# Kernel tuning notes

Hardware: AMD Instinct MI355X
Metric: run time of the kernel (lower is better)

The kernel has to match this reference:

```python
import jax, jax.numpy as jnp
import numpy as np
from jax import lax

NH = 1024
CATS = 1024
B = 64
T = 512


def setup_inputs() -> dict:
    key = jax.random.key(0)
    ks = jax.random.split(key, 12)
    s_in = 1.0 / np.sqrt(CATS)
    s_h = 1.0 / np.sqrt(NH)
    return {
        "x": jax.random.normal(ks[0], (B, T, CATS), jnp.float32),
        "h0": jax.random.normal(ks[1], (B, NH), jnp.float32),
        # torch Linear weights are [out, in]
        "Wh": jax.random.uniform(ks[2], (NH, CATS), jnp.float32, -s_in, s_in),
        "Wz": jax.random.uniform(ks[3], (NH, CATS), jnp.float32, -s_in, s_in),
        "Wr": jax.random.uniform(ks[4], (NH, CATS), jnp.float32, -s_in, s_in),
        "Uh": jax.random.uniform(ks[5], (NH, NH), jnp.float32, -s_h, s_h),
        "Uz": jax.random.uniform(ks[6], (NH, NH), jnp.float32, -s_h, s_h),
        "Ur": jax.random.uniform(ks[7], (NH, NH), jnp.float32, -s_h, s_h),
        "bz": jax.random.uniform(ks[8], (NH,), jnp.float32, -s_h, s_h),
        "br": jax.random.uniform(ks[9], (NH,), jnp.float32, -s_h, s_h),
        "Wout": jax.random.uniform(ks[10], (CATS, NH), jnp.float32, -s_h, s_h),
    }


def _gru_last_h(x, h0, Wh, Wz, Wr, Uh, Uz, Ur, bz, br):
    # Precompute input projections as big GEMMs: [B,T,nh] each
    xh = jnp.einsum('btc,hc->bth', x, Wh)
    xz = jnp.einsum('btc,hc->bth', x, Wz)
    # Note: reset gate r is computed in the original but NEVER used in htilde
    # (htilde = tanh(Wh x + Uh h)); it does not affect the output, so we omit it.
    # Scan over time: inputs as [T, B, nh]
    seq = (jnp.swapaxes(xh, 0, 1), jnp.swapaxes(xz, 0, 1))

    def step(h, inp):
        xh_t, xz_t = inp
        z = jax.nn.sigmoid(xz_t + h @ Uz.T + bz)
        htilde = jnp.tanh(xh_t + h @ Uh.T)
        h_new = (1.0 - z) * h + z * htilde
        return h_new, None

    hT, _ = lax.scan(step, h0, seq)
    return hT  # [B, nh]


def reference(x, h0, Wh, Wz, Wr, Uh, Uz, Ur, bz, br, Wout):
    hT = _gru_last_h(x, h0, Wh, Wz, Wr, Uh, Uz, Ur, bz, br)
    return hT @ Wout.T  # [B, cats]
```

## Files before the change

### kernel.cpp

```cpp
#include <hip/hip_runtime.h>

typedef __attribute__((ext_vector_type(8))) short short8v;
typedef __attribute__((ext_vector_type(4))) float f32x4;
typedef __attribute__((ext_vector_type(4))) float float4v;
typedef unsigned long long u64;

#define NHID 1024
#define NCAT 1024
#define NB   64
#define NT   512
#define RING_STRIDE 65536

__device__ __forceinline__ short f2bf(float f) {
  union { float f; unsigned u; } c; c.f = f;
  unsigned r = (c.u + 0x7fffu + ((c.u >> 16) & 1u)) >> 16;
  return (short)r;
}

__device__ __forceinline__ void ast(u64* p, u64 v) {
  __hip_atomic_store(p, v, __ATOMIC_RELAXED, __HIP_MEMORY_SCOPE_AGENT);
}

__device__ __forceinline__ short8v cvt8(float4v a, float4v b) {
  short8v s;
  s[0]=f2bf(a[0]); s[1]=f2bf(a[1]); s[2]=f2bf(a[2]); s[3]=f2bf(a[3]);
  s[4]=f2bf(b[0]); s[5]=f2bf(b[1]); s[6]=f2bf(b[2]); s[7]=f2bf(b[3]);
  return s;
}

__global__ __launch_bounds__(256, 1) void gru_kernel(
    const float* __restrict__ h0, const float* __restrict__ Wh, const float* __restrict__ Wz,
    const float* __restrict__ Uh, const float* __restrict__ Uz, const float* __restrict__ bz,
    const float* __restrict__ Wout, const float* __restrict__ x,
    short* __restrict__ ring, unsigned* __restrict__ flags, float* __restrict__ out)
{
  extern __shared__ char smem[];
  short8v* ufr = (short8v*)smem;
  float*   red = (float*)(smem + 131072);
  short*   rp  = (short*)(smem + 131072 + 12288);

  __builtin_amdgcn_fence(__ATOMIC_ACQUIRE, "agent");

  const int tid  = threadIdx.x;
  const int lane = tid & 63;
  const int wv   = tid >> 6;
  const int mt   = blockIdx.x >> 6;
  const int cg   = blockIdx.x & 63;
  const int col  = lane & 15;
  const int quad = lane >> 4;
  const int kq   = quad * 8;
  const int jg   = cg * 16 + col;

  for (int idx = tid; idx < 64 * 2 * 64; idx += 256) {
    int l  = idx & 63;
    int nt = (idx >> 6) & 1;
    int kb = idx >> 7;
    int j  = cg * 16 + (l & 15);
    int k0 = (kb & 31) * 32 + (l >> 4) * 8;
    const float* M = (kb < 32) ? (nt ? Uh : Uz) : (nt ? Wh : Wz);
    short8v v;
#pragma unroll
    for (int e = 0; e < 8; ++e) v[e] = f2bf(M[j * 1024 + k0 + e]);
    ufr[idx] = v;
  }
  __syncthreads();

  float hl[4] = {0.f, 0.f, 0.f, 0.f};
  float bzv = 0.f;
  if (wv == 0) {
    bzv = bz[jg];
#pragma unroll
    for (int r = 0; r < 4; ++r) hl[r] = h0[(mt * 16 + quad * 4 + r) * NHID + jg];
  }

  const int kb0 = wv * 16;
  unsigned* myflag = flags + (mt * 64 + cg) * 16;
  const unsigned* pollp  = flags + (mt * 64 + (wv & 1) * 32 + (lane & 31)) * 16;
  const unsigned* pollpt = flags + (mt * 64 + wv * 16 + (lane & 15)) * 16;

  short8v xf[16];
  if (wv >= 2) {
    const float* xrow = x + ((long)(mt * 16 + col) * NT + 0) * NCAT + (kb0 - 32) * 32 + kq;
#pragma unroll
    for (int i = 0; i < 16; ++i)
      xf[i] = cvt8(*(const float4v*)(xrow + i * 32), *(const float4v*)(xrow + i * 32 + 4));
  }

  for (int t = 0; t < NT; ++t) {
    const int par = t & 1;
    f32x4 pz = {0.f,0.f,0.f,0.f}, ph = {0.f,0.f,0.f,0.f};

    if (wv < 2) {
      short8v f[16];
      if (t > 0) {
        const unsigned tt = (unsigned)t;
        for (;;) {
          unsigned v = __hip_atomic_load(pollp, __ATOMIC_RELAXED, __HIP_MEMORY_SCOPE_AGENT);
          if (__ballot(v < tt) == 0ull) break;
          __builtin_amdgcn_s_sleep(1);
        }
        __asm__ volatile("" ::: "memory");
        const short* hrow = ring + (size_t)t * RING_STRIDE
                          + (mt * 16 + col) * 1024 + kb0 * 32 + kq;
#pragma unroll
        for (int i = 0; i < 16; ++i) f[i] = *(const short8v*)(hrow + i * 32);
      } else {
        const float* hrow = h0 + (mt * 16 + col) * NHID + kb0 * 32 + kq;
#pragma unroll
        for (int i = 0; i < 16; ++i)
          f[i] = cvt8(*(const float4v*)(hrow + i * 32), *(const float4v*)(hrow + i * 32 + 4));
      }
#pragma unroll
      for (int i = 0; i < 16; ++i) {
        int kb = kb0 + i;
        pz = __builtin_amdgcn_mfma_f32_16x16x32_bf16(f[i], ufr[kb * 128 + lane],      pz, 0, 0, 0);
        ph = __builtin_amdgcn_mfma_f32_16x16x32_bf16(f[i], ufr[kb * 128 + 64 + lane], ph, 0, 0, 0);
      }
    } else {
#pragma unroll
      for (int i = 0; i < 16; ++i) {
        int kb = kb0 + i;
        pz = __builtin_amdgcn_mfma_f32_16x16x32_bf16(xf[i], ufr[kb * 128 + lane],      pz, 0, 0, 0);
        ph = __builtin_amdgcn_mfma_f32_16x16x32_bf16(xf[i], ufr[kb * 128 + 64 + lane], ph, 0, 0, 0);
      }
      if (t + 1 < NT) {
        const float* xrow = x + ((long)(mt * 16 + col) * NT + (t + 1)) * NCAT + (kb0 - 32) * 32 + kq;
#pragma unroll
        for (int i = 0; i < 16; ++i)
          xf[i] = cvt8(*(const float4v*)(xrow + i * 32), *(const float4v*)(xrow + i * 32 + 4));
      }
    }

    if (wv != 0) {
      float* sl = red + ((par * 3 + (wv - 1)) * 64 + lane) * 8;
      *(f32x4*)sl       = pz;
      *(f32x4*)(sl + 4) = ph;
    }
    __syncthreads();

    if (wv == 0) {
      f32x4 accz = pz, acch = ph;
#pragma unroll
      for (int s = 0; s < 3; ++s) {
        const float* sl = red + ((par * 3 + s) * 64 + lane) * 8;
        accz += *(const f32x4*)sl;
        acch += *(const f32x4*)(sl + 4);
      }
#pragma unroll
      for (int r = 0; r < 4; ++r) {
        float zp = accz[r] + bzv;
        float z  = 1.f / (1.f + __expf(-zp));
        float ht = 2.f / (1.f + __expf(-2.f * acch[r])) - 1.f;
        float v  = hl[r] + z * (ht - hl[r]);
        hl[r] = v;
        rp[(quad * 4 + r) * 16 + col] = f2bf(v);
      }
      __asm__ volatile("s_waitcnt lgkmcnt(0)" ::: "memory");
      u64 val = ((const u64*)rp)[lane];
      u64* hnq = (u64*)(ring + (size_t)(t + 1) * RING_STRIDE);
      ast(hnq + (mt * 16 + (lane >> 2)) * 256 + cg * 4 + (lane & 3), val);
      __asm__ volatile("s_waitcnt vmcnt(0)" ::: "memory");
      if (lane == 0)
        __hip_atomic_store(myflag, (unsigned)(t + 1), __ATOMIC_RELAXED, __HIP_MEMORY_SCOPE_AGENT);
    }
  }

  {
    for (;;) {
      unsigned v = __hip_atomic_load(pollpt, __ATOMIC_RELAXED, __HIP_MEMORY_SCOPE_AGENT);
      if (__ballot(v < (unsigned)NT) == 0ull) break;
      __builtin_amdgcn_s_sleep(1);
    }
    __asm__ volatile("" ::: "memory");
    const int kb0t = wv * 8;
    const short* hrow = ring + (size_t)NT * RING_STRIDE
                      + (mt * 16 + col) * 1024 + kb0t * 32 + kq;
    f32x4 acc = {0.f,0.f,0.f,0.f};
    const float* wrow = Wout + (long)jg * NHID + kb0t * 32 + kq;
#pragma unroll
    for (int kb = 0; kb < 8; ++kb) {
      short8v a = *(const short8v*)(hrow + kb * 32);
      float4v w0 = *(const float4v*)(wrow + kb * 32);
      float4v w1 = *(const float4v*)(wrow + kb * 32 + 4);
      acc = __builtin_amdgcn_mfma_f32_16x16x32_bf16(a, cvt8(w0, w1), acc, 0, 0, 0);
    }
    if (wv != 0)
      *(f32x4*)(red + ((wv - 1) * 64 + lane) * 8) = acc;
    __syncthreads();
    if (wv == 0) {
#pragma unroll
      for (int s = 0; s < 3; ++s)
        acc += *(const f32x4*)(red + (s * 64 + lane) * 8);
#pragma unroll
      for (int r = 0; r < 4; ++r)
        out[(mt * 16 + quad * 4 + r) * NCAT + jg] = acc[r];
    }
  }
}

extern "C" void kernel_launch(void* const* d_in, const int* in_sizes, int n_in,
                              void* d_out, int out_size, void* d_ws, size_t ws_size,
                              hipStream_t stream) {
  const float* x    = (const float*)d_in[0];
  const float* h0   = (const float*)d_in[1];
  const float* Wh   = (const float*)d_in[2];
  const float* Wz   = (const float*)d_in[3];
  const float* Uh   = (const float*)d_in[5];
  const float* Uz   = (const float*)d_in[6];
  const float* bz   = (const float*)d_in[8];
  const float* Wout = (const float*)d_in[10];

  char* ws = (char*)d_ws;
  unsigned* flags = (unsigned*)ws;
  short* ring = (short*)(ws + 16384);

  hipMemsetAsync(flags, 0, 16384, stream);

  hipFuncSetAttribute((const void*)gru_kernel,
                      hipFuncAttributeMaxDynamicSharedMemorySize, 143872);
  gru_kernel<<<256, 256, 143872, stream>>>(h0, Wh, Wz, Uh, Uz, bz, Wout, x,
                                           ring, flags, (float*)d_out);
}
```

Before: 2.384 ms.

## Split recurrent and input K-range evenly across all four waves per step

Each of the four waves now handles 8 recurrent-state K blocks and 8 input K blocks, where before two waves did the whole recurrent half and two did the input half. The critical path after each flag wait shrinks to 8 ring loads and 16 MFMAs per wave. The gate epilogue is spread over all 256 threads, each computing one element and storing one bf16 directly to the ring, followed by a block barrier and a single flag store. The s_sleep in the polling loops is removed, and the next x tile is prefetched after the flag is published. The cost is an extra barrier per step and narrow 2-byte atomic stores in place of packed 8-byte stores.

```diff
diff --git a/kernel.cpp b/kernel.cpp
--- a/kernel.cpp
+++ b/kernel.cpp
@@ -15,10 +15,6 @@
   union { float f; unsigned u; } c; c.f = f;
   unsigned r = (c.u + 0x7fffu + ((c.u >> 16) & 1u)) >> 16;
   return (short)r;
-}
-
-__device__ __forceinline__ void ast(u64* p, u64 v) {
-  __hip_atomic_store(p, v, __ATOMIC_RELAXED, __HIP_MEMORY_SCOPE_AGENT);
 }
 
 __device__ __forceinline__ short8v cvt8(float4v a, float4v b) {
@@ -37,7 +33,6 @@
   extern __shared__ char smem[];
   short8v* ufr = (short8v*)smem;
   float*   red = (float*)(smem + 131072);
-  short*   rp  = (short*)(smem + 131072 + 12288);
 
   __builtin_amdgcn_fence(__ATOMIC_ACQUIRE, "agent");
 
@@ -49,7 +44,9 @@
   const int col  = lane & 15;
   const int quad = lane >> 4;
   const int kq   = quad * 8;
-  const int jg   = cg * 16 + col;
+  const int row_t = tid >> 4;
+  const int col_t = tid & 15;
+  const int jg_t  = cg * 16 + col_t;
 
   for (int idx = tid; idx < 64 * 2 * 64; idx += 256) {
     int l  = idx & 63;
@@ -65,118 +62,98 @@
   }
   __syncthreads();
 
-  float hl[4] = {0.f, 0.f, 0.f, 0.f};
-  float bzv = 0.f;
-  if (wv == 0) {
-    bzv = bz[jg];
-#pragma unroll
-    for (int r = 0; r < 4; ++r) hl[r] = h0[(mt * 16 + quad * 4 + r) * NHID + jg];
-  }
-
-  const int kb0 = wv * 16;
+  float hl  = h0[(mt * 16 + row_t) * NHID + jg_t];
+  const float bzv = bz[jg_t];
+
+  const int kb0h = wv * 8;
+  const int kb0x = 32 + wv * 8;
   unsigned* myflag = flags + (mt * 64 + cg) * 16;
-  const unsigned* pollp  = flags + (mt * 64 + (wv & 1) * 32 + (lane & 31)) * 16;
-  const unsigned* pollpt = flags + (mt * 64 + wv * 16 + (lane & 15)) * 16;
-
-  short8v xf[16];
-  if (wv >= 2) {
-    const float* xrow = x + ((long)(mt * 16 + col) * NT + 0) * NCAT + (kb0 - 32) * 32 + kq;
-#pragma unroll
-    for (int i = 0; i < 16; ++i)
+  const unsigned* pollp = flags + (mt * 64 + wv * 16 + (lane & 15)) * 16;
+
+  short8v xf[8];
+  {
+    const float* xrow = x + ((long)(mt * 16 + col) * NT + 0) * NCAT + (kb0x - 32) * 32 + kq;
+#pragma unroll
+    for (int i = 0; i < 8; ++i)
       xf[i] = cvt8(*(const float4v*)(xrow + i * 32), *(const float4v*)(xrow + i * 32 + 4));
   }
 
   for (int t = 0; t < NT; ++t) {
-    const int par = t & 1;
+    short8v hf[8];
+    if (t > 0) {
+      const unsigned tt = (unsigned)t;
+      for (;;) {
+        unsigned v = __hip_atomic_load(pollp, __ATOMIC_RELAXED, __HIP_MEMORY_SCOPE_AGENT);
+        if (__ballot(v < tt) == 0ull) break;
+      }
+      __asm__ volatile("" ::: "memory");
+      const short* hrow = ring + (size_t)t * RING_STRIDE
+                        + (mt * 16 + col) * 1024 + kb0h * 32 + kq;
+#pragma unroll
+      for (int i = 0; i < 8; ++i) hf[i] = *(const short8v*)(hrow + i * 32);
+    } else {
+      const float* hrow = h0 + (mt * 16 + col) * NHID + kb0h * 32 + kq;
+#pragma unroll
+      for (int i = 0; i < 8; ++i)
+        hf[i] = cvt8(*(const float4v*)(hrow + i * 32), *(const float4v*)(hrow + i * 32 + 4));
+    }
+
     f32x4 pz = {0.f,0.f,0.f,0.f}, ph = {0.f,0.f,0.f,0.f};
-
-    if (wv < 2) {
-      short8v f[16];
-      if (t > 0) {
-        const unsigned tt = (unsigned)t;
-        for (;;) {
-          unsigned v = __hip_atomic_load(pollp, __ATOMIC_RELAXED, __HIP_MEMORY_SCOPE_AGENT);
-          if (__ballot(v < tt) == 0ull) break;
-          __builtin_amdgcn_s_sleep(1);
-        }
-        __asm__ volatile("" ::: "memory");
-        const short* hrow = ring + (size_t)t * RING_STRIDE
-                          + (mt * 16 + col) * 1024 + kb0 * 32 + kq;
-#pragma unroll
-        for (int i = 0; i < 16; ++i) f[i] = *(const short8v*)(hrow + i * 32);
-      } else {
-        const float* hrow = h0 + (mt * 16 + col) * NHID + kb0 * 32 + kq;
-#pragma unroll
-        for (int i = 0; i < 16; ++i)
-          f[i] = cvt8(*(const float4v*)(hrow + i * 32), *(const float4v*)(hrow + i * 32 + 4));
-      }
-#pragma unroll
-      for (int i = 0; i < 16; ++i) {
-        int kb = kb0 + i;
-        pz = __builtin_amdgcn_mfma_f32_16x16x32_bf16(f[i], ufr[kb * 128 + lane],      pz, 0, 0, 0);
-        ph = __builtin_amdgcn_mfma_f32_16x16x32_bf16(f[i], ufr[kb * 128 + 64 + lane], ph, 0, 0, 0);
-      }
-    } else {
-#pragma unroll
-      for (int i = 0; i < 16; ++i) {
-        int kb = kb0 + i;
-        pz = __builtin_amdgcn_mfma_f32_16x16x32_bf16(xf[i], ufr[kb * 128 + lane],      pz, 0, 0, 0);
-        ph = __builtin_amdgcn_mfma_f32_16x16x32_bf16(xf[i], ufr[kb * 128 + 64 + lane], ph, 0, 0, 0);
-      }
-      if (t + 1 < NT) {
-        const float* xrow = x + ((long)(mt * 16 + col) * NT + (t + 1)) * NCAT + (kb0 - 32) * 32 + kq;
-#pragma unroll
-        for (int i = 0; i < 16; ++i)
-          xf[i] = cvt8(*(const float4v*)(xrow + i * 32), *(const float4v*)(xrow + i * 32 + 4));
-      }
-    }
-
-    if (wv != 0) {
-      float* sl = red + ((par * 3 + (wv - 1)) * 64 + lane) * 8;
-      *(f32x4*)sl       = pz;
-      *(f32x4*)(sl + 4) = ph;
-    }
+#pragma unroll
+    for (int i = 0; i < 8; ++i) {
+      int kb = kb0h + i;
+      pz = __builtin_amdgcn_mfma_f32_16x16x32_bf16(hf[i], ufr[kb * 128 + lane],      pz, 0, 0, 0);
+      ph = __builtin_amdgcn_mfma_f32_16x16x32_bf16(hf[i], ufr[kb * 128 + 64 + lane], ph, 0, 0, 0);
+    }
+#pragma unroll
+    for (int i = 0; i < 8; ++i) {
+      int kb = kb0x + i;
+      pz = __builtin_amdgcn_mfma_f32_16x16x32_bf16(xf[i], ufr[kb * 128 + lane],      pz, 0, 0, 0);
+      ph = __builtin_amdgcn_mfma_f32_16x16x32_bf16(xf[i], ufr[kb * 128 + 64 + lane], ph, 0, 0, 0);
+    }
+
+    ((f32x4*)red)[(wv * 2 + 0) * 64 + lane] = pz;
+    ((f32x4*)red)[(wv * 2 + 1) * 64 + lane] = ph;
     __syncthreads();
 
-    if (wv == 0) {
-      f32x4 accz = pz, acch = ph;
-#pragma unroll
-      for (int s = 0; s < 3; ++s) {
-        const float* sl = red + ((par * 3 + s) * 64 + lane) * 8;
-        accz += *(const f32x4*)sl;
-        acch += *(const f32x4*)(sl + 4);
-      }
-#pragma unroll
-      for (int r = 0; r < 4; ++r) {
-        float zp = accz[r] + bzv;
-        float z  = 1.f / (1.f + __expf(-zp));
-        float ht = 2.f / (1.f + __expf(-2.f * acch[r])) - 1.f;
-        float v  = hl[r] + z * (ht - hl[r]);
-        hl[r] = v;
-        rp[(quad * 4 + r) * 16 + col] = f2bf(v);
-      }
-      __asm__ volatile("s_waitcnt lgkmcnt(0)" ::: "memory");
-      u64 val = ((const u64*)rp)[lane];
-      u64* hnq = (u64*)(ring + (size_t)(t + 1) * RING_STRIDE);
-      ast(hnq + (mt * 16 + (lane >> 2)) * 256 + cg * 4 + (lane & 3), val);
-      __asm__ volatile("s_waitcnt vmcnt(0)" ::: "memory");
-      if (lane == 0)
-        __hip_atomic_store(myflag, (unsigned)(t + 1), __ATOMIC_RELAXED, __HIP_MEMORY_SCOPE_AGENT);
+    {
+      const int idx = 4 * ((row_t >> 2) * 16 + col_t) + (row_t & 3);
+      float accz = red[idx] + red[512 + idx] + red[1024 + idx] + red[1536 + idx];
+      float acch = red[256 + idx] + red[768 + idx] + red[1280 + idx] + red[1792 + idx];
+      float zp = accz + bzv;
+      float z  = 1.f / (1.f + __expf(-zp));
+      float ht = 2.f / (1.f + __expf(-2.f * acch)) - 1.f;
+      float v  = hl + z * (ht - hl);
+      hl = v;
+      unsigned short* dst = (unsigned short*)(ring + (size_t)(t + 1) * RING_STRIDE
+                                              + (mt * 16 + row_t) * 1024 + jg_t);
+      __hip_atomic_store(dst, (unsigned short)f2bf(v),
+                         __ATOMIC_RELAXED, __HIP_MEMORY_SCOPE_AGENT);
+    }
+    __asm__ volatile("s_waitcnt vmcnt(0)" ::: "memory");
+    __syncthreads();
+    if (tid == 0)
+      __hip_atomic_store(myflag, (unsigned)(t + 1), __ATOMIC_RELAXED, __HIP_MEMORY_SCOPE_AGENT);
+
+    if (t + 1 < NT) {
+      const float* xrow = x + ((long)(mt * 16 + col) * NT + (t + 1)) * NCAT + (kb0x - 32) * 32 + kq;
+#pragma unroll
+      for (int i = 0; i < 8; ++i)
+        xf[i] = cvt8(*(const float4v*)(xrow + i * 32), *(const float4v*)(xrow + i * 32 + 4));
     }
   }
 
   {
     for (;;) {
-      unsigned v = __hip_atomic_load(pollpt, __ATOMIC_RELAXED, __HIP_MEMORY_SCOPE_AGENT);
+      unsigned v = __hip_atomic_load(pollp, __ATOMIC_RELAXED, __HIP_MEMORY_SCOPE_AGENT);
       if (__ballot(v < (unsigned)NT) == 0ull) break;
-      __builtin_amdgcn_s_sleep(1);
     }
     __asm__ volatile("" ::: "memory");
-    const int kb0t = wv * 8;
+    const int jg = cg * 16 + col;
     const short* hrow = ring + (size_t)NT * RING_STRIDE
-                      + (mt * 16 + col) * 1024 + kb0t * 32 + kq;
+                      + (mt * 16 + col) * 1024 + kb0h * 32 + kq;
     f32x4 acc = {0.f,0.f,0.f,0.f};
-    const float* wrow = Wout + (long)jg * NHID + kb0t * 32 + kq;
+    const float* wrow = Wout + (long)jg * NHID + kb0h * 32 + kq;
 #pragma unroll
     for (int kb = 0; kb < 8; ++kb) {
       short8v a = *(const short8v*)(hrow + kb * 32);
@@ -185,12 +162,12 @@
       acc = __builtin_amdgcn_mfma_f32_16x16x32_bf16(a, cvt8(w0, w1), acc, 0, 0, 0);
     }
     if (wv != 0)
-      *(f32x4*)(red + ((wv - 1) * 64 + lane) * 8) = acc;
+      ((f32x4*)red)[(wv - 1) * 64 + lane] = acc;
     __syncthreads();
     if (wv == 0) {
 #pragma unroll
       for (int s = 0; s < 3; ++s)
-        acc += *(const f32x4*)(red + (s * 64 + lane) * 8);
+        acc += ((const f32x4*)red)[s * 64 + lane];
 #pragma unroll
       for (int r = 0; r < 4; ++r)
         out[(mt * 16 + quad * 4 + r) * NCAT + jg] = acc[r];
@@ -217,7 +194,7 @@
   hipMemsetAsync(flags, 0, 16384, stream);
 
   hipFuncSetAttribute((const void*)gru_kernel,
-                      hipFuncAttributeMaxDynamicSharedMemorySize, 143872);
-  gru_kernel<<<256, 256, 143872, stream>>>(h0, Wh, Wz, Uh, Uz, bz, Wout, x,
+                      hipFuncAttributeMaxDynamicSharedMemorySize, 139264);
+  gru_kernel<<<256, 256, 139264, stream>>>(h0, Wh, Wz, Uh, Uz, bz, Wout, x,
                                            ring, flags, (float*)d_out);
 }
```

Result: slower. 3.733 ms (+56.6%).

## Move gate epilogue and publish to x-waves, split MFMA accumulator chains

Applied to the files above, without the earlier changes.

The per-step reduction and gate/update epilogue moves off wave 0 and onto waves 2 and 3, the x-projection waves that never poll. Each of those waves handles 8 rows, publishes its half of the new hidden state, and sets its own flag word. Pollers now check two flag words per block. Each wave also splits its MFMA accumulation into two independent chains to shorten the dependency latency, and the next x prefetch is issued after the publish. The aim is a shorter critical path from the reduction to the ring write. The cost is a larger shared-memory reduction buffer and twice as many flag polls per step.

```diff
diff --git a/kernel.cpp b/kernel.cpp
--- a/kernel.cpp
+++ b/kernel.cpp
@@ -15,10 +15,6 @@
   union { float f; unsigned u; } c; c.f = f;
   unsigned r = (c.u + 0x7fffu + ((c.u >> 16) & 1u)) >> 16;
   return (short)r;
-}
-
-__device__ __forceinline__ void ast(u64* p, u64 v) {
-  __hip_atomic_store(p, v, __ATOMIC_RELAXED, __HIP_MEMORY_SCOPE_AGENT);
 }
 
 __device__ __forceinline__ short8v cvt8(float4v a, float4v b) {
@@ -37,7 +33,7 @@
   extern __shared__ char smem[];
   short8v* ufr = (short8v*)smem;
   float*   red = (float*)(smem + 131072);
-  short*   rp  = (short*)(smem + 131072 + 12288);
+  short*   rp  = (short*)(smem + 131072 + 16384);
 
   __builtin_amdgcn_fence(__ATOMIC_ACQUIRE, "agent");
 
@@ -49,7 +45,6 @@
   const int col  = lane & 15;
   const int quad = lane >> 4;
   const int kq   = quad * 8;
-  const int jg   = cg * 16 + col;
 
   for (int idx = tid; idx < 64 * 2 * 64; idx += 256) {
     int l  = idx & 63;
@@ -65,18 +60,21 @@
   }
   __syncthreads();
 
-  float hl[4] = {0.f, 0.f, 0.f, 0.f};
+  const int w    = wv - 2;
+  const int r0   = (wv >= 2) ? (w * 8 + (lane >> 4) * 2) : 0;
+  const int jg_e = cg * 16 + col;
+  float hl[2] = {0.f, 0.f};
   float bzv = 0.f;
-  if (wv == 0) {
-    bzv = bz[jg];
-#pragma unroll
-    for (int r = 0; r < 4; ++r) hl[r] = h0[(mt * 16 + quad * 4 + r) * NHID + jg];
+  if (wv >= 2) {
+    bzv = bz[jg_e];
+    hl[0] = h0[(mt * 16 + r0)     * NHID + jg_e];
+    hl[1] = h0[(mt * 16 + r0 + 1) * NHID + jg_e];
   }
 
   const int kb0 = wv * 16;
-  unsigned* myflag = flags + (mt * 64 + cg) * 16;
-  const unsigned* pollp  = flags + (mt * 64 + (wv & 1) * 32 + (lane & 31)) * 16;
-  const unsigned* pollpt = flags + (mt * 64 + wv * 16 + (lane & 15)) * 16;
+  unsigned* flagline = flags + (mt * 64 + cg) * 16;
+  const unsigned* pollp  = flags + (mt * 64 + (wv & 1) * 32 + (lane >> 1)) * 16 + (lane & 1);
+  const unsigned* pollpt = flags + (mt * 64 + wv * 16 + ((lane >> 1) & 15)) * 16 + (lane & 1);
 
   short8v xf[16];
   if (wv >= 2) {
@@ -88,7 +86,9 @@
 
   for (int t = 0; t < NT; ++t) {
     const int par = t & 1;
-    f32x4 pz = {0.f,0.f,0.f,0.f}, ph = {0.f,0.f,0.f,0.f};
+    float* redp = red + par * 2048;
+    f32x4 pz0 = {0.f,0.f,0.f,0.f}, pz1 = {0.f,0.f,0.f,0.f};
+    f32x4 ph0 = {0.f,0.f,0.f,0.f}, ph1 = {0.f,0.f,0.f,0.f};
 
     if (wv < 2) {
       short8v f[16];
@@ -111,57 +111,65 @@
           f[i] = cvt8(*(const float4v*)(hrow + i * 32), *(const float4v*)(hrow + i * 32 + 4));
       }
 #pragma unroll
-      for (int i = 0; i < 16; ++i) {
+      for (int i = 0; i < 16; i += 2) {
         int kb = kb0 + i;
-        pz = __builtin_amdgcn_mfma_f32_16x16x32_bf16(f[i], ufr[kb * 128 + lane],      pz, 0, 0, 0);
-        ph = __builtin_amdgcn_mfma_f32_16x16x32_bf16(f[i], ufr[kb * 128 + 64 + lane], ph, 0, 0, 0);
+        pz0 = __builtin_amdgcn_mfma_f32_16x16x32_bf16(f[i],   ufr[kb * 128 + lane],        pz0, 0, 0, 0);
+        ph0 = __builtin_amdgcn_mfma_f32_16x16x32_bf16(f[i],   ufr[kb * 128 + 64 + lane],   ph0, 0, 0, 0);
+        pz1 = __builtin_amdgcn_mfma_f32_16x16x32_bf16(f[i+1], ufr[(kb+1) * 128 + lane],    pz1, 0, 0, 0);
+        ph1 = __builtin_amdgcn_mfma_f32_16x16x32_bf16(f[i+1], ufr[(kb+1) * 128 + 64 + lane], ph1, 0, 0, 0);
       }
     } else {
 #pragma unroll
-      for (int i = 0; i < 16; ++i) {
+      for (int i = 0; i < 16; i += 2) {
         int kb = kb0 + i;
-        pz = __builtin_amdgcn_mfma_f32_16x16x32_bf16(xf[i], ufr[kb * 128 + lane],      pz, 0, 0, 0);
-        ph = __builtin_amdgcn_mfma_f32_16x16x32_bf16(xf[i], ufr[kb * 128 + 64 + lane], ph, 0, 0, 0);
-      }
+        pz0 = __builtin_amdgcn_mfma_f32_16x16x32_bf16(xf[i],   ufr[kb * 128 + lane],        pz0, 0, 0, 0);
+        ph0 = __builtin_amdgcn_mfma_f32_16x16x32_bf16(xf[i],   ufr[kb * 128 + 64 + lane],   ph0, 0, 0, 0);
+        pz1 = __builtin_amdgcn_mfma_f32_16x16x32_bf16(xf[i+1], ufr[(kb+1) * 128 + lane],    pz1, 0, 0, 0);
+        ph1 = __builtin_amdgcn_mfma_f32_16x16x32_bf16(xf[i+1], ufr[(kb+1) * 128 + 64 + lane], ph1, 0, 0, 0);
+      }
+    }
+
+    ((f32x4*)redp)[(wv * 2 + 0) * 64 + lane] = pz0 + pz1;
+    ((f32x4*)redp)[(wv * 2 + 1) * 64 + lane] = ph0 + ph1;
+    __syncthreads();
+
+    if (wv >= 2) {
+      float vv[2];
+#pragma unroll
+      for (int r = 0; r < 2; ++r) {
+        int row = r0 + r;
+        int ls  = ((row >> 2) << 4) | col;
+        int reg = row & 3;
+        float accz = redp[(0*2+0)*256 + ls*4 + reg] + redp[(1*2+0)*256 + ls*4 + reg]
+                   + redp[(2*2+0)*256 + ls*4 + reg] + redp[(3*2+0)*256 + ls*4 + reg];
+        float acch = redp[(0*2+1)*256 + ls*4 + reg] + redp[(1*2+1)*256 + ls*4 + reg]
+                   + redp[(2*2+1)*256 + ls*4 + reg] + redp[(3*2+1)*256 + ls*4 + reg];
+        float zp = accz + bzv;
+        float z  = 1.f / (1.f + __expf(-zp));
+        float ht = 2.f / (1.f + __expf(-2.f * acch)) - 1.f;
+        float v  = hl[r] + z * (ht - hl[r]);
+        hl[r] = v; vv[r] = v;
+      }
+      rp[w * 128 + (r0 & 7) * 16 + col]       = f2bf(vv[0]);
+      rp[w * 128 + ((r0 + 1) & 7) * 16 + col] = f2bf(vv[1]);
+      __asm__ volatile("s_waitcnt lgkmcnt(0)" ::: "memory");
+      if (lane < 32) {
+        u64 val = ((const u64*)(rp + w * 128))[lane];
+        int row = w * 8 + (lane >> 2);
+        u64* dst = (u64*)(ring + (size_t)(t + 1) * RING_STRIDE
+                          + (mt * 16 + row) * 1024 + cg * 16) + (lane & 3);
+        __hip_atomic_store(dst, val, __ATOMIC_RELAXED, __HIP_MEMORY_SCOPE_AGENT);
+      }
+      __asm__ volatile("s_waitcnt vmcnt(0)" ::: "memory");
+      if (lane == 0)
+        __hip_atomic_store(flagline + w, (unsigned)(t + 1),
+                           __ATOMIC_RELAXED, __HIP_MEMORY_SCOPE_AGENT);
       if (t + 1 < NT) {
         const float* xrow = x + ((long)(mt * 16 + col) * NT + (t + 1)) * NCAT + (kb0 - 32) * 32 + kq;
 #pragma unroll
         for (int i = 0; i < 16; ++i)
           xf[i] = cvt8(*(const float4v*)(xrow + i * 32), *(const float4v*)(xrow + i * 32 + 4));
       }
-    }
-
-    if (wv != 0) {
-      float* sl = red + ((par * 3 + (wv - 1)) * 64 + lane) * 8;
-      *(f32x4*)sl       = pz;
-      *(f32x4*)(sl + 4) = ph;
-    }
-    __syncthreads();
-
-    if (wv == 0) {
-      f32x4 accz = pz, acch = ph;
-#pragma unroll
-      for (int s = 0; s < 3; ++s) {
-        const float* sl = red + ((par * 3 + s) * 64 + lane) * 8;
-        accz += *(const f32x4*)sl;
-        acch += *(const f32x4*)(sl + 4);
-      }
-#pragma unroll
-      for (int r = 0; r < 4; ++r) {
-        float zp = accz[r] + bzv;
-        float z  = 1.f / (1.f + __expf(-zp));
-        float ht = 2.f / (1.f + __expf(-2.f * acch[r])) - 1.f;
-        float v  = hl[r] + z * (ht - hl[r]);
-        hl[r] = v;
-        rp[(quad * 4 + r) * 16 + col] = f2bf(v);
-      }
-      __asm__ volatile("s_waitcnt lgkmcnt(0)" ::: "memory");
-      u64 val = ((const u64*)rp)[lane];
-      u64* hnq = (u64*)(ring + (size_t)(t + 1) * RING_STRIDE);
-      ast(hnq + (mt * 16 + (lane >> 2)) * 256 + cg * 4 + (lane & 3), val);
-      __asm__ volatile("s_waitcnt vmcnt(0)" ::: "memory");
-      if (lane == 0)
-        __hip_atomic_store(myflag, (unsigned)(t + 1), __ATOMIC_RELAXED, __HIP_MEMORY_SCOPE_AGENT);
     }
   }
 
@@ -172,6 +180,7 @@
       __builtin_amdgcn_s_sleep(1);
     }
     __asm__ volatile("" ::: "memory");
+    const int jg = cg * 16 + col;
     const int kb0t = wv * 8;
     const short* hrow = ring + (size_t)NT * RING_STRIDE
                       + (mt * 16 + col) * 1024 + kb0t * 32 + kq;
@@ -185,12 +194,12 @@
       acc = __builtin_amdgcn_mfma_f32_16x16x32_bf16(a, cvt8(w0, w1), acc, 0, 0, 0);
     }
     if (wv != 0)
-      *(f32x4*)(red + ((wv - 1) * 64 + lane) * 8) = acc;
+      ((f32x4*)red)[(wv - 1) * 64 + lane] = acc;
     __syncthreads();
     if (wv == 0) {
 #pragma unroll
       for (int s = 0; s < 3; ++s)
-        acc += *(const f32x4*)(red + (s * 64 + lane) * 8);
+        acc += ((const f32x4*)red)[s * 64 + lane];
 #pragma unroll
       for (int r = 0; r < 4; ++r)
         out[(mt * 16 + quad * 4 + r) * NCAT + jg] = acc[r];
@@ -217,7 +226,7 @@
   hipMemsetAsync(flags, 0, 16384, stream);
 
   hipFuncSetAttribute((const void*)gru_kernel,
-                      hipFuncAttributeMaxDynamicSharedMemorySize, 143872);
-  gru_kernel<<<256, 256, 143872, stream>>>(h0, Wh, Wz, Uh, Uz, bz, Wout, x,
+                      hipFuncAttributeMaxDynamicSharedMemorySize, 147968);
+  gru_kernel<<<256, 256, 147968, stream>>>(h0, Wh, Wz, Uh, Uz, bz, Wout, x,
                                            ring, flags, (float*)d_out);
 }
```

Result: slower. 2.499 ms (+4.8%).
